# Kernel tuning notes

Measured on AMD Instinct MI355X. Metric: run time of the kernel, lower is better.

The kernel has to match this reference:

```python
import jax, jax.numpy as jnp
import numpy as np

N = 50000       # nodes
E = 800000      # edges
IN = 256        # input channels
H = 4           # heads
C = 64          # hidden channels per head
NEG_SLOPE = 0.2 # PyG GATConv default LeakyReLU slope
EPS = 1e-16


def setup_inputs() -> dict:
    key = jax.random.key(0)
    k_x, k_e, k_w, k_as, k_ad = jax.random.split(key, 5)
    x = jax.random.normal(k_x, (N, IN), dtype=jnp.float32)
    edge_index = jax.random.randint(k_e, (2, E), 0, N, dtype=jnp.int64)
    # GATConv params: glorot-style scale
    W = jax.random.normal(k_w, (IN, H * C), dtype=jnp.float32) * (1.0 / np.sqrt(IN))
    att_src = jax.random.normal(k_as, (H, C), dtype=jnp.float32) * (1.0 / np.sqrt(C))
    att_dst = jax.random.normal(k_ad, (H, C), dtype=jnp.float32) * (1.0 / np.sqrt(C))
    return {"x": x, "edge_index": edge_index, "W": W, "att_src": att_src, "att_dst": att_dst}


def reference(x, edge_index, W, att_src, att_dst):
    src, dst = edge_index[0], edge_index[1]
    # linear projection, split heads: [N, H, C]
    xh = (x @ W).reshape(N, H, C)
    # per-node attention halves: [N, H]
    a_src = jnp.einsum('nhc,hc->nh', xh, att_src)
    a_dst = jnp.einsum('nhc,hc->nh', xh, att_dst)
    # per-edge logits with LeakyReLU: [E, H]
    alpha = a_src[src] + a_dst[dst]
    alpha = jnp.where(alpha >= 0, alpha, NEG_SLOPE * alpha)
    # segment softmax over destination nodes
    m = jax.ops.segment_max(alpha, dst, num_segments=N)          # [N, H]
    ex = jnp.exp(alpha - m[dst])                                  # [E, H]
    denom = jax.ops.segment_sum(ex, dst, num_segments=N)         # [N, H]
    att = ex / (denom[dst] + EPS)                                 # [E, H]
    # weighted message scatter-add: [N, H, C] -> concat heads [N, H*C]
    msg = att[:, :, None] * xh[src]                               # [E, H, C]
    out = jax.ops.segment_sum(msg, dst, num_segments=N)
    out = out.reshape(N, H * C)
    return (out, att)
```

## Files before the change

### kernel.cpp

```cpp
#include <hip/hip_runtime.h>
#include <math.h>

#define IN_CH   256
#define HC      256
#define H_HEADS 4
#define NEG_SLOPE 0.2f
#define LOG2E   1.44269504088896f
#define DEFER_THR 12.0f
#define MINIT   -3.0e38f

typedef __attribute__((ext_vector_type(8))) short short8;
typedef __attribute__((ext_vector_type(4))) short short4v;
typedef __attribute__((ext_vector_type(4))) float float4v;

__device__ __forceinline__ float bf2f(unsigned short b) {
    return __uint_as_float(((unsigned)b) << 16);
}
__device__ __forceinline__ unsigned short f2bf(float f) {
    unsigned u = __float_as_uint(f);
    u += 0x7fffu + ((u >> 16) & 1u);
    return (unsigned short)(u >> 16);
}
__device__ __forceinline__ float lrelu(float a) {
    return a >= 0.f ? a : NEG_SLOPE * a;
}
__device__ __forceinline__ float fexp2(float a) {
    return __builtin_amdgcn_exp2f(a);
}


__global__ void prep_w(const float* __restrict__ w,
                       unsigned short* __restrict__ wt) {
    int idx = blockIdx.x * 256 + threadIdx.x;
    int k = idx >> 8, c = idx & 255;
    wt[(size_t)c * 256 + k] = f2bf(w[idx]);
}

__global__ __launch_bounds__(256) void gemm_xh(const float* __restrict__ x,
                                               const unsigned short* __restrict__ wt,
                                               const float* __restrict__ att_s,
                                               const float* __restrict__ att_d,
                                               unsigned short* __restrict__ xh_bf,
                                               float* __restrict__ a_src,
                                               float* __restrict__ a_dst, int N) {
    __shared__ __attribute__((aligned(16))) unsigned char lds_a[16384];
    int tid  = threadIdx.x;
    int wave = tid >> 6;
    int lane = tid & 63;
    int quad = lane >> 4;
    int l16  = lane & 15;
    int rb   = blockIdx.x * 16;

#pragma unroll
    for (int pass = 0; pass < 2; ++pass) {
        int s  = pass * 256 + tid;
        int kc = s >> 4;
        int m  = s & 15;
        int grow = rb + m; if (grow >= N) grow = N - 1;
        const float* gp = x + (size_t)grow * IN_CH + kc * 8;
        float4v f0 = *(const float4v*)gp;
        float4v f1 = *(const float4v*)(gp + 4);
        short8 hi, lo;
#pragma unroll
        for (int j = 0; j < 4; ++j) {
            unsigned short h0 = f2bf(f0[j]);
            hi[j] = (short)h0;
            lo[j] = (short)f2bf(f0[j] - bf2f(h0));
            unsigned short h1 = f2bf(f1[j]);
            hi[4 + j] = (short)h1;
            lo[4 + j] = (short)f2bf(f1[j] - bf2f(h1));
        }
        *(short8*)(lds_a + (size_t)s * 16) = hi;
        *(short8*)(lds_a + 8192 + (size_t)s * 16) = lo;
    }
    __syncthreads();

    float4v acc[4] = {};
    const unsigned short* wt_base = wt + ((size_t)wave * 64 + l16) * IN_CH;
#pragma unroll
    for (int k0 = 0; k0 < 8; ++k0) {
        int kc   = k0 * 4 + quad;
        int slot = kc * 16 + l16;
        short8 a_hi = *(const short8*)(lds_a + slot * 16);
        short8 a_lo = *(const short8*)(lds_a + 8192 + slot * 16);
#pragma unroll
        for (int ct = 0; ct < 4; ++ct) {
            short8 bh = *(const short8*)(wt_base + (size_t)ct * 16 * IN_CH
                                         + k0 * 32 + quad * 8);
            acc[ct] = __builtin_amdgcn_mfma_f32_16x16x32_bf16(a_lo, bh, acc[ct], 0, 0, 0);
            acc[ct] = __builtin_amdgcn_mfma_f32_16x16x32_bf16(a_hi, bh, acc[ct], 0, 0, 0);
        }
    }

    int cb = wave;
    float ps[4] = {0.f, 0.f, 0.f, 0.f};
    float pd[4] = {0.f, 0.f, 0.f, 0.f};
#pragma unroll
    for (int ct = 0; ct < 4; ++ct) {
        float as_c = att_s[cb * 64 + ct * 16 + l16] * LOG2E;
        float ad_c = att_d[cb * 64 + ct * 16 + l16] * LOG2E;
#pragma unroll
        for (int r = 0; r < 4; ++r) {
            float v = acc[ct][r];
            int grow = rb + quad * 4 + r;
            if (grow < N)
                xh_bf[(size_t)grow * HC + cb * 64 + ct * 16 + l16] = f2bf(v);
            ps[r] += v * as_c;
            pd[r] += v * ad_c;
        }
    }
#pragma unroll
    for (int off = 1; off < 16; off <<= 1) {
#pragma unroll
        for (int r = 0; r < 4; ++r) {
            ps[r] += __shfl_xor(ps[r], off);
            pd[r] += __shfl_xor(pd[r], off);
        }
    }
    if (l16 == 0) {
#pragma unroll
        for (int r = 0; r < 4; ++r) {
            int grow = rb + quad * 4 + r;
            if (grow < N) {
                a_src[(size_t)grow * 4 + cb] = ps[r];
                a_dst[(size_t)grow * 4 + cb] = pd[r];
            }
        }
    }
}

__global__ __launch_bounds__(256) void deg_count(const int* __restrict__ ei,
                                                 int* __restrict__ deg, int E) {
    int e = blockIdx.x * 256 + threadIdx.x;
    if (e >= E) return;
    atomicAdd(deg + ei[E + e], 1);
}


__global__ __launch_bounds__(256) void scan_part(const int* __restrict__ deg,
                                                 int* __restrict__ part, int N) {
    int t = threadIdx.x;
    int base = blockIdx.x * 1024 + t * 4;
    int s = 0;
    if (base + 4 <= N) {
        int4 v = *(const int4*)(deg + base);
        s = v.x + v.y + v.z + v.w;
    } else {
#pragma unroll
        for (int j = 0; j < 4; ++j)
            if (base + j < N) s += deg[base + j];
    }
#pragma unroll
    for (int off = 1; off < 64; off <<= 1) s += __shfl_xor(s, off);
    __shared__ int ws[4];
    if ((t & 63) == 0) ws[t >> 6] = s;
    __syncthreads();
    if (t == 0) part[blockIdx.x] = ws[0] + ws[1] + ws[2] + ws[3];
}

__global__ __launch_bounds__(256) void scan_final(const int* __restrict__ deg,
                                                  const int* __restrict__ part,
                                                  int* __restrict__ rowptr,
                                                  int* __restrict__ cursor, int N) {
    __shared__ int sm[256];
    __shared__ int wsum[4];
    int t = threadIdx.x;
    int bacc = 0;
    for (int j = t; j < blockIdx.x; j += 256) bacc += part[j];
#pragma unroll
    for (int off = 1; off < 64; off <<= 1) bacc += __shfl_xor(bacc, off);
    if ((t & 63) == 0) wsum[t >> 6] = bacc;

    int base = blockIdx.x * 1024 + t * 4;
    int v0 = 0, v1 = 0, v2 = 0, v3 = 0;
    if (base + 4 <= N) {
        int4 v = *(const int4*)(deg + base);
        v0 = v.x; v1 = v.y; v2 = v.z; v3 = v.w;
    } else {
        if (base + 0 < N) v0 = deg[base + 0];
        if (base + 1 < N) v1 = deg[base + 1];
        if (base + 2 < N) v2 = deg[base + 2];
        if (base + 3 < N) v3 = deg[base + 3];
    }
    int s = v0 + v1 + v2 + v3;
    sm[t] = s;
    __syncthreads();
    for (int off = 1; off < 256; off <<= 1) {
        int tmp = (t >= off) ? sm[t - off] : 0;
        __syncthreads();
        sm[t] += tmp;
        __syncthreads();
    }
    int boff = wsum[0] + wsum[1] + wsum[2] + wsum[3];
    int run = boff + sm[t] - s;
    int r0 = run, r1 = r0 + v0, r2 = r1 + v1, r3 = r2 + v2;
    if (base + 4 <= N) {
        *(int4*)(rowptr + base) = (int4){r0, r1, r2, r3};
        *(int4*)(cursor + base) = (int4){r0, r1, r2, r3};
    } else {
        if (base + 0 < N) { rowptr[base + 0] = r0; cursor[base + 0] = r0; }
        if (base + 1 < N) { rowptr[base + 1] = r1; cursor[base + 1] = r1; }
        if (base + 2 < N) { rowptr[base + 2] = r2; cursor[base + 2] = r2; }
        if (base + 3 < N) { rowptr[base + 3] = r3; cursor[base + 3] = r3; }
    }
}

__global__ __launch_bounds__(256) void fill_csr(const int* __restrict__ ei,
                                                const float* __restrict__ a_src,
                                                const float* __restrict__ a_dst,
                                                int* __restrict__ cursor,
                                                int* __restrict__ csr_off,
                                                float* __restrict__ csr_al, int E) {
    int e = blockIdx.x * 256 + threadIdx.x;
    if (e >= E) return;
    int s = ei[e], d = ei[E + e];
    float4v as = *(const float4v*)(a_src + (size_t)s * 4);
    float4v ad = *(const float4v*)(a_dst + (size_t)d * 4);
    float4v al;
#pragma unroll
    for (int h = 0; h < 4; ++h) al[h] = lrelu(as[h] + ad[h]);
    int slot = atomicAdd(cursor + d, 1);
    csr_off[slot] = s << 9;
    *(float4v*)(csr_al + (size_t)slot * 4) = al;
}

__global__ __launch_bounds__(256) void gat_gather(const int* __restrict__ csr_off,
                                                  const float* __restrict__ csr_al,
                                                  const int* __restrict__ rowptr,
                                                  const int* __restrict__ deg,
                                                  const unsigned short* __restrict__ xh_bf,
                                                  float* __restrict__ out,
                                                  float* __restrict__ pack, int N) {
    int wave = threadIdx.x >> 6, lane = threadIdx.x & 63;
    int half = lane >> 5;
    int l32  = lane & 31;
    int h    = l32 >> 3;
    int d    = blockIdx.x * 8 + wave * 2 + half;
    bool dv  = d < N;
    int dc   = dv ? d : N - 1;
    int start = rowptr[dc];
    int cnt   = dv ? deg[dc] : 0;
    int cntMax = max(cnt, __shfl_xor(cnt, 32));

    const char* xb = (const char*)xh_bf;
    int lboff = l32 * 16;

    float mE = MINIT, lE = 0.f, mO = MINIT, lO = 0.f;
    float accE[8] = {0.f, 0.f, 0.f, 0.f, 0.f, 0.f, 0.f, 0.f};
    float accO[8] = {0.f, 0.f, 0.f, 0.f, 0.f, 0.f, 0.f, 0.f};

#define LOFF(idx) (((idx) < cnt) ? csr_off[start + (idx)] : 0)
#define LAL(idx)  (((idx) < cnt) ? csr_al[(size_t)(start + (idx)) * 4 + h] : -INFINITY)

    int o4 = LOFF(4), o5 = LOFF(5);
    float alE  = LAL(0), alO  = LAL(1);
    float alE1 = LAL(2), alO1 = LAL(3);
    short8 xvE  = *(const short8*)(xb + (size_t)(unsigned)LOFF(0) + lboff);
    short8 xvO  = *(const short8*)(xb + (size_t)(unsigned)LOFF(1) + lboff);
    short8 xvE1 = *(const short8*)(xb + (size_t)(unsigned)LOFF(2) + lboff);
    short8 xvO1 = *(const short8*)(xb + (size_t)(unsigned)LOFF(3) + lboff);

#pragma unroll 2
    for (int i = 0; i < cntMax; i += 2) {
        short8 xvE2 = *(const short8*)(xb + (size_t)(unsigned)o4 + lboff);
        short8 xvO2 = *(const short8*)(xb + (size_t)(unsigned)o5 + lboff);
        int o6 = LOFF(i + 6), o7 = LOFF(i + 7);
        float alE2 = LAL(i + 4), alO2 = LAL(i + 5);

        bool ok = (alE <= mE + DEFER_THR) && (alO <= mO + DEFER_THR);
        if (__all(ok)) {
            float p = fexp2(alE - mE);
            float q = fexp2(alO - mO);
            lE += p; lO += q;
#pragma unroll
            for (int j = 0; j < 8; ++j) {
                accE[j] += p * bf2f((unsigned short)xvE[j]);
                accO[j] += q * bf2f((unsigned short)xvO[j]);
            }
        } else {
            float mnE = fmaxf(mE, alE);
            float scE = fexp2(mE - mnE);
            float pE  = fexp2(alE - mnE);
            lE = lE * scE + pE;
            float mnO = fmaxf(mO, alO);
            float scO = fexp2(mO - mnO);
            float pO  = fexp2(alO - mnO);
            lO = lO * scO + pO;
#pragma unroll
            for (int j = 0; j < 8; ++j) {
                accE[j] = accE[j] * scE + pE * bf2f((unsigned short)xvE[j]);
                accO[j] = accO[j] * scO + pO * bf2f((unsigned short)xvO[j]);
            }
            mE = mnE; mO = mnO;
        }
        alE = alE1; alO = alO1; alE1 = alE2; alO1 = alO2;
        xvE = xvE1; xvO = xvO1; xvE1 = xvE2; xvO1 = xvO2;
        o4 = o6; o5 = o7;
    }
#undef LOFF
#undef LAL

    float mm = fmaxf(mE, mO);
    float sE = fexp2(mE - mm), sO = fexp2(mO - mm);
    float l  = lE * sE + lO * sO;
    float inv = 1.f / (l + 1e-16f);
    if (dv) {
        float4v o0, o1;
#pragma unroll
        for (int j = 0; j < 4; ++j) {
            o0[j] = (accE[j] * sE + accO[j] * sO) * inv;
            o1[j] = (accE[4 + j] * sE + accO[4 + j] * sO) * inv;
        }
        float* orow = out + (size_t)d * HC + l32 * 8;
        *(float4v*)orow = o0;
        *(float4v*)(orow + 4) = o1;
        if ((l32 & 7) == 0) {
            pack[(size_t)d * 8 + h]     = mm;
            pack[(size_t)d * 8 + 4 + h] = inv;
        }
    }
}

__global__ __launch_bounds__(256) void att_edge(const int* __restrict__ ei,
                                                const float* __restrict__ a_src,
                                                const float* __restrict__ a_dst,
                                                const float* __restrict__ pack,
                                                float* __restrict__ att_out, int E) {
    int e = blockIdx.x * 256 + threadIdx.x;
    if (e >= E) return;
    int s = ei[e], d = ei[E + e];
    float4v as = *(const float4v*)(a_src + (size_t)s * 4);
    float4v ad = *(const float4v*)(a_dst + (size_t)d * 4);
    float4v mm = *(const float4v*)(pack + (size_t)d * 8);
    float4v gg = *(const float4v*)(pack + (size_t)d * 8 + 4);
    float4v o;
#pragma unroll
    for (int h = 0; h < 4; ++h)
        o[h] = fexp2(lrelu(as[h] + ad[h]) - mm[h]) * gg[h];
    *(float4v*)(att_out + (size_t)e * 4) = o;
}

extern "C" void kernel_launch(void* const* d_in, const int* in_sizes, int n_in,
                              void* d_out, int out_size, void* d_ws, size_t ws_size,
                              hipStream_t stream) {
    const float* x     = (const float*)d_in[0];
    const int*   ei    = (const int*)d_in[1];
    const float* W     = (const float*)d_in[2];
    const float* att_s = (const float*)d_in[3];
    const float* att_d = (const float*)d_in[4];

    const int N = in_sizes[0] / IN_CH;
    const int E = in_sizes[1] / 2;

    char* ws = (char*)d_ws;
    size_t off = 0;
    unsigned short* xh_bf = (unsigned short*)(ws + off); off += (size_t)N * HC * 2;
    unsigned short* wt    = (unsigned short*)(ws + off); off += (size_t)IN_CH * HC * 2;
    float* a_src = (float*)(ws + off); off += (size_t)N * H_HEADS * 4;
    float* a_dst = (float*)(ws + off); off += (size_t)N * H_HEADS * 4;
    float* pack  = (float*)(ws + off); off += (size_t)N * 8 * 4;
    int* rowptr  = (int*)(ws + off); off += (size_t)N * 4;
    int* cursor  = (int*)(ws + off); off += (size_t)N * 4;
    int* csr_off = (int*)(ws + off); off += (size_t)E * 4;
    float* csr_al = (float*)(ws + off); off += (size_t)E * 4 * 4;
    int* part    = (int*)(ws + off); off += 1024 * 4;
    size_t zoff = off;
    int* deg     = (int*)(ws + off); off += (size_t)N * 4;

    float* out     = (float*)d_out;
    float* out_att = out + (size_t)N * HC;

    (void)hipMemsetAsync(ws + zoff, 0, off - zoff, stream);

    const int NB = (N + 1023) / 1024;

    prep_w<<<256, 256, 0, stream>>>(W, wt);
    deg_count<<<(E + 255) / 256, 256, 0, stream>>>(ei, deg, E);
    gemm_xh<<<(N + 15) / 16, 256, 0, stream>>>(x, wt, att_s, att_d,
                                               xh_bf, a_src, a_dst, N);
    scan_part<<<NB, 256, 0, stream>>>(deg, part, N);
    scan_final<<<NB, 256, 0, stream>>>(deg, part, rowptr, cursor, N);
    fill_csr<<<(E + 255) / 256, 256, 0, stream>>>(ei, a_src, a_dst, cursor,
                                                  csr_off, csr_al, E);
    gat_gather<<<(N + 7) / 8, 256, 0, stream>>>(csr_off, csr_al, rowptr, deg,
                                                xh_bf, out, pack, N);
    att_edge<<<(E + 255) / 256, 256, 0, stream>>>(ei, a_src, a_dst, pack,
                                                  out_att, E);
}
```

Measured before the change: 329.9 us.

## Split xh into 32-channel planes and precompute softmax stats before gather

Stores the projected features as eight planes of 32 channels each, so every gather block touches one 3.2 MB plane that fits better in cache. A separate per-node, per-head pass computes the softmax max and normalizer, which lets the gather drop its online-softmax rescaling. Edge logits move to a head-major layout. The cost is an extra kernel, and each edge's index and logit are now read eight times, once per plane block, with 4-byte gathers instead of 16-byte ones.

```diff
diff --git a/kernel.cpp b/kernel.cpp
--- a/kernel.cpp
+++ b/kernel.cpp
@@ -6,12 +6,11 @@
 #define H_HEADS 4
 #define NEG_SLOPE 0.2f
 #define LOG2E   1.44269504088896f
-#define DEFER_THR 12.0f
 #define MINIT   -3.0e38f
 
 typedef __attribute__((ext_vector_type(8))) short short8;
-typedef __attribute__((ext_vector_type(4))) short short4v;
 typedef __attribute__((ext_vector_type(4))) float float4v;
+typedef __attribute__((ext_vector_type(2))) float float2v;
 
 __device__ __forceinline__ float bf2f(unsigned short b) {
     return __uint_as_float(((unsigned)b) << 16);
@@ -40,7 +39,7 @@
                                                const unsigned short* __restrict__ wt,
                                                const float* __restrict__ att_s,
                                                const float* __restrict__ att_d,
-                                               unsigned short* __restrict__ xh_bf,
+                                               unsigned short* __restrict__ xh_pl,
                                                float* __restrict__ a_src,
                                                float* __restrict__ a_dst, int N) {
     __shared__ __attribute__((aligned(16))) unsigned char lds_a[16384];
@@ -99,12 +98,14 @@
     for (int ct = 0; ct < 4; ++ct) {
         float as_c = att_s[cb * 64 + ct * 16 + l16] * LOG2E;
         float ad_c = att_d[cb * 64 + ct * 16 + l16] * LOG2E;
+        int ch = cb * 64 + ct * 16 + l16;
+        int pl = ch >> 5, wc = ch & 31;
 #pragma unroll
         for (int r = 0; r < 4; ++r) {
             float v = acc[ct][r];
             int grow = rb + quad * 4 + r;
             if (grow < N)
-                xh_bf[(size_t)grow * HC + cb * 64 + ct * 16 + l16] = f2bf(v);
+                xh_pl[((size_t)pl * N + grow) * 32 + wc] = f2bf(v);
             ps[r] += v * as_c;
             pd[r] += v * ad_c;
         }
@@ -135,7 +136,6 @@
     if (e >= E) return;
     atomicAdd(deg + ei[E + e], 1);
 }
-
 
 __global__ __launch_bounds__(256) void scan_part(const int* __restrict__ deg,
                                                  int* __restrict__ part, int N) {
@@ -209,115 +209,104 @@
                                                 const float* __restrict__ a_src,
                                                 const float* __restrict__ a_dst,
                                                 int* __restrict__ cursor,
-                                                int* __restrict__ csr_off,
+                                                int* __restrict__ csr_off6,
                                                 float* __restrict__ csr_al, int E) {
     int e = blockIdx.x * 256 + threadIdx.x;
     if (e >= E) return;
     int s = ei[e], d = ei[E + e];
     float4v as = *(const float4v*)(a_src + (size_t)s * 4);
     float4v ad = *(const float4v*)(a_dst + (size_t)d * 4);
-    float4v al;
-#pragma unroll
-    for (int h = 0; h < 4; ++h) al[h] = lrelu(as[h] + ad[h]);
     int slot = atomicAdd(cursor + d, 1);
-    csr_off[slot] = s << 9;
-    *(float4v*)(csr_al + (size_t)slot * 4) = al;
-}
-
-__global__ __launch_bounds__(256) void gat_gather(const int* __restrict__ csr_off,
+    csr_off6[slot] = s << 6;
+#pragma unroll
+    for (int h = 0; h < 4; ++h)
+        csr_al[(size_t)h * E + slot] = lrelu(as[h] + ad[h]);
+}
+
+__global__ __launch_bounds__(256) void softmax_stats(const float* __restrict__ csr_al,
+                                                     const int* __restrict__ rowptr,
+                                                     const int* __restrict__ deg,
+                                                     float* __restrict__ pack,
+                                                     int N, int E) {
+    int d = blockIdx.x * 256 + threadIdx.x;
+    int h = blockIdx.y;
+    if (d >= N) return;
+    int start = rowptr[d], cnt = deg[d];
+    const float* alh = csr_al + (size_t)h * E + start;
+    float m = MINIT, l = 0.f;
+    for (int i = 0; i < cnt; ++i) {
+        float al = alh[i];
+        float mn = fmaxf(m, al);
+        l = l * fexp2(m - mn) + fexp2(al - mn);
+        m = mn;
+    }
+    pack[(size_t)d * 8 + h]     = m;
+    pack[(size_t)d * 8 + 4 + h] = 1.f / (l + 1e-16f);
+}
+
+__global__ __launch_bounds__(256) void gat_planes(const int* __restrict__ csr_off6,
                                                   const float* __restrict__ csr_al,
                                                   const int* __restrict__ rowptr,
                                                   const int* __restrict__ deg,
-                                                  const unsigned short* __restrict__ xh_bf,
-                                                  float* __restrict__ out,
-                                                  float* __restrict__ pack, int N) {
-    int wave = threadIdx.x >> 6, lane = threadIdx.x & 63;
-    int half = lane >> 5;
-    int l32  = lane & 31;
-    int h    = l32 >> 3;
-    int d    = blockIdx.x * 8 + wave * 2 + half;
-    bool dv  = d < N;
-    int dc   = dv ? d : N - 1;
+                                                  const unsigned short* __restrict__ xh_pl,
+                                                  const float* __restrict__ pack,
+                                                  float* __restrict__ out, int N, int E) {
+    int tid = threadIdx.x;
+    int g   = blockIdx.x & 7;
+    int db  = blockIdx.x >> 3;
+    int grp = tid >> 4;
+    int l16 = tid & 15;
+    int d   = db * 16 + grp;
+    bool dv = d < N;
+    int dc  = dv ? d : N - 1;
     int start = rowptr[dc];
     int cnt   = dv ? deg[dc] : 0;
-    int cntMax = max(cnt, __shfl_xor(cnt, 32));
-
-    const char* xb = (const char*)xh_bf;
-    int lboff = l32 * 16;
-
-    float mE = MINIT, lE = 0.f, mO = MINIT, lO = 0.f;
-    float accE[8] = {0.f, 0.f, 0.f, 0.f, 0.f, 0.f, 0.f, 0.f};
-    float accO[8] = {0.f, 0.f, 0.f, 0.f, 0.f, 0.f, 0.f, 0.f};
-
-#define LOFF(idx) (((idx) < cnt) ? csr_off[start + (idx)] : 0)
-#define LAL(idx)  (((idx) < cnt) ? csr_al[(size_t)(start + (idx)) * 4 + h] : -INFINITY)
-
-    int o4 = LOFF(4), o5 = LOFF(5);
-    float alE  = LAL(0), alO  = LAL(1);
-    float alE1 = LAL(2), alO1 = LAL(3);
-    short8 xvE  = *(const short8*)(xb + (size_t)(unsigned)LOFF(0) + lboff);
-    short8 xvO  = *(const short8*)(xb + (size_t)(unsigned)LOFF(1) + lboff);
-    short8 xvE1 = *(const short8*)(xb + (size_t)(unsigned)LOFF(2) + lboff);
-    short8 xvO1 = *(const short8*)(xb + (size_t)(unsigned)LOFF(3) + lboff);
+    int h = g >> 1;
+
+    int cw = cnt;
+    cw = max(cw, __shfl_xor(cw, 16));
+    cw = max(cw, __shfl_xor(cw, 32));
+
+    const float* alh = csr_al + (size_t)h * E;
+    const char* pb = (const char*)xh_pl + (size_t)g * N * 64;
+    int lb = l16 * 4;
+    float m   = pack[(size_t)dc * 8 + h];
+    float inv = pack[(size_t)dc * 8 + 4 + h];
+
+    float aE0 = 0.f, aE1 = 0.f, aO0 = 0.f, aO1 = 0.f;
+
+#define POFF(i) (((i) < cnt) ? csr_off6[start + (i)] : 0)
+#define PAL(i)  (((i) < cnt) ? alh[start + (i)] : -INFINITY)
+
+    int oE = POFF(0), oO = POFF(1);
+    float alE = PAL(0), alO = PAL(1);
+    int oE1 = POFF(2), oO1 = POFF(3);
 
 #pragma unroll 2
-    for (int i = 0; i < cntMax; i += 2) {
-        short8 xvE2 = *(const short8*)(xb + (size_t)(unsigned)o4 + lboff);
-        short8 xvO2 = *(const short8*)(xb + (size_t)(unsigned)o5 + lboff);
-        int o6 = LOFF(i + 6), o7 = LOFF(i + 7);
-        float alE2 = LAL(i + 4), alO2 = LAL(i + 5);
-
-        bool ok = (alE <= mE + DEFER_THR) && (alO <= mO + DEFER_THR);
-        if (__all(ok)) {
-            float p = fexp2(alE - mE);
-            float q = fexp2(alO - mO);
-            lE += p; lO += q;
-#pragma unroll
-            for (int j = 0; j < 8; ++j) {
-                accE[j] += p * bf2f((unsigned short)xvE[j]);
-                accO[j] += q * bf2f((unsigned short)xvO[j]);
-            }
-        } else {
-            float mnE = fmaxf(mE, alE);
-            float scE = fexp2(mE - mnE);
-            float pE  = fexp2(alE - mnE);
-            lE = lE * scE + pE;
-            float mnO = fmaxf(mO, alO);
-            float scO = fexp2(mO - mnO);
-            float pO  = fexp2(alO - mnO);
-            lO = lO * scO + pO;
-#pragma unroll
-            for (int j = 0; j < 8; ++j) {
-                accE[j] = accE[j] * scE + pE * bf2f((unsigned short)xvE[j]);
-                accO[j] = accO[j] * scO + pO * bf2f((unsigned short)xvO[j]);
-            }
-            mE = mnE; mO = mnO;
-        }
-        alE = alE1; alO = alO1; alE1 = alE2; alO1 = alO2;
-        xvE = xvE1; xvO = xvO1; xvE1 = xvE2; xvO1 = xvO2;
-        o4 = o6; o5 = o7;
-    }
-#undef LOFF
-#undef LAL
-
-    float mm = fmaxf(mE, mO);
-    float sE = fexp2(mE - mm), sO = fexp2(mO - mm);
-    float l  = lE * sE + lO * sO;
-    float inv = 1.f / (l + 1e-16f);
+    for (int i = 0; i < cw; i += 2) {
+        unsigned xE = *(const unsigned*)(pb + (size_t)(unsigned)oE + lb);
+        unsigned xO = *(const unsigned*)(pb + (size_t)(unsigned)oO + lb);
+        int oE2 = POFF(i + 4), oO2 = POFF(i + 5);
+        float alEn = PAL(i + 2), alOn = PAL(i + 3);
+
+        float pE = fexp2(alE - m);
+        float pO = fexp2(alO - m);
+        aE0 += pE * bf2f((unsigned short)(xE & 0xffffu));
+        aE1 += pE * bf2f((unsigned short)(xE >> 16));
+        aO0 += pO * bf2f((unsigned short)(xO & 0xffffu));
+        aO1 += pO * bf2f((unsigned short)(xO >> 16));
+
+        oE = oE1; oO = oO1; oE1 = oE2; oO1 = oO2;
+        alE = alEn; alO = alOn;
+    }
+#undef POFF
+#undef PAL
+
     if (dv) {
-        float4v o0, o1;
-#pragma unroll
-        for (int j = 0; j < 4; ++j) {
-            o0[j] = (accE[j] * sE + accO[j] * sO) * inv;
-            o1[j] = (accE[4 + j] * sE + accO[4 + j] * sO) * inv;
-        }
-        float* orow = out + (size_t)d * HC + l32 * 8;
-        *(float4v*)orow = o0;
-        *(float4v*)(orow + 4) = o1;
-        if ((l32 & 7) == 0) {
-            pack[(size_t)d * 8 + h]     = mm;
-            pack[(size_t)d * 8 + 4 + h] = inv;
-        }
+        float2v o;
+        o[0] = (aE0 + aO0) * inv;
+        o[1] = (aE1 + aO1) * inv;
+        *(float2v*)(out + (size_t)d * HC + g * 32 + l16 * 2) = o;
     }
 }
 
@@ -354,14 +343,14 @@
 
     char* ws = (char*)d_ws;
     size_t off = 0;
-    unsigned short* xh_bf = (unsigned short*)(ws + off); off += (size_t)N * HC * 2;
+    unsigned short* xh_pl = (unsigned short*)(ws + off); off += (size_t)N * HC * 2;
     unsigned short* wt    = (unsigned short*)(ws + off); off += (size_t)IN_CH * HC * 2;
     float* a_src = (float*)(ws + off); off += (size_t)N * H_HEADS * 4;
     float* a_dst = (float*)(ws + off); off += (size_t)N * H_HEADS * 4;
     float* pack  = (float*)(ws + off); off += (size_t)N * 8 * 4;
     int* rowptr  = (int*)(ws + off); off += (size_t)N * 4;
     int* cursor  = (int*)(ws + off); off += (size_t)N * 4;
-    int* csr_off = (int*)(ws + off); off += (size_t)E * 4;
+    int* csr_off6 = (int*)(ws + off); off += (size_t)E * 4;
     float* csr_al = (float*)(ws + off); off += (size_t)E * 4 * 4;
     int* part    = (int*)(ws + off); off += 1024 * 4;
     size_t zoff = off;
@@ -372,18 +361,21 @@
 
     (void)hipMemsetAsync(ws + zoff, 0, off - zoff, stream);
 
-    const int NB = (N + 1023) / 1024;
+    const int NB  = (N + 1023) / 1024;
+    const int NDB = (N + 15) / 16;
 
     prep_w<<<256, 256, 0, stream>>>(W, wt);
     deg_count<<<(E + 255) / 256, 256, 0, stream>>>(ei, deg, E);
     gemm_xh<<<(N + 15) / 16, 256, 0, stream>>>(x, wt, att_s, att_d,
-                                               xh_bf, a_src, a_dst, N);
+                                               xh_pl, a_src, a_dst, N);
     scan_part<<<NB, 256, 0, stream>>>(deg, part, N);
     scan_final<<<NB, 256, 0, stream>>>(deg, part, rowptr, cursor, N);
     fill_csr<<<(E + 255) / 256, 256, 0, stream>>>(ei, a_src, a_dst, cursor,
-                                                  csr_off, csr_al, E);
-    gat_gather<<<(N + 7) / 8, 256, 0, stream>>>(csr_off, csr_al, rowptr, deg,
-                                                xh_bf, out, pack, N);
+                                                  csr_off6, csr_al, E);
+    softmax_stats<<<dim3((N + 255) / 256, 4), 256, 0, stream>>>(csr_al, rowptr, deg,
+                                                                pack, N, E);
+    gat_planes<<<NDB * 8, 256, 0, stream>>>(csr_off6, csr_al, rowptr, deg,
+                                            xh_pl, pack, out, N, E);
     att_edge<<<(E + 255) / 256, 256, 0, stream>>>(ei, a_src, a_dst, pack,
                                                   out_att, E);
 }
```

Measured after the change: 364.2 us. +10.4%, slower.
